# Kernel tuning notes

Hardware: AMD Instinct MI355X
Metric: run time of the kernel (lower is better)

Reference implementation:

```python
import jax, jax.numpy as jnp
import numpy as np

DIM = 512
NUM_HEADS = 8
HEAD_DIM = DIM // NUM_HEADS
FFN_DIM = 4 * DIM
EPS = 1e-6


def rmsnorm(x, w):
    rms = jnp.sqrt(jnp.mean(x * x, axis=-1, keepdims=True) + EPS)
    return x / rms * w


def setup_inputs() -> dict:
    key = jax.random.key(0)
    ks = jax.random.split(key, 8)
    B, T = 4, 2048
    x = jax.random.normal(ks[0], (B, T, DIM), dtype=jnp.float32)
    # Linear weights stored as [in, out] (transpose of torch layout)
    w_qkv = jax.random.normal(ks[1], (DIM, 3 * DIM), dtype=jnp.float32) * 0.02
    w_out = jax.random.normal(ks[2], (DIM, DIM), dtype=jnp.float32) * 0.02
    b_out = jnp.zeros((DIM,), dtype=jnp.float32)
    w1 = jax.random.normal(ks[3], (DIM, FFN_DIM), dtype=jnp.float32) * 0.02
    b1 = jnp.zeros((FFN_DIM,), dtype=jnp.float32)
    w2 = jax.random.normal(ks[4], (FFN_DIM, DIM), dtype=jnp.float32) * 0.02
    b2 = jnp.zeros((DIM,), dtype=jnp.float32)
    norm1_w = jnp.ones((DIM,), dtype=jnp.float32)
    norm2_w = jnp.ones((DIM,), dtype=jnp.float32)
    return {
        "x": x, "norm1_w": norm1_w, "norm2_w": norm2_w,
        "w_qkv": w_qkv, "w_out": w_out, "b_out": b_out,
        "w1": w1, "b1": b1, "w2": w2, "b2": b2,
        "context_size": 64,
    }


def reference(x, norm1_w, norm2_w, w_qkv, w_out, b_out, w1, b1, w2, b2, context_size):
    B, T, D = x.shape
    H, Hd = NUM_HEADS, HEAD_DIM
    # --- attention sublayer ---
    xn = rmsnorm(x, norm1_w)
    qkv = xn @ w_qkv                      # (B, T, 3D)
    q, k, v = jnp.split(qkv, 3, axis=-1)
    q = q.reshape(B, T, H, Hd).transpose(0, 2, 1, 3)  # (B, H, T, Hd)
    k = k.reshape(B, T, H, Hd).transpose(0, 2, 1, 3)
    v = v.reshape(B, T, H, Hd).transpose(0, 2, 1, 3)
    scale = Hd ** -0.5
    scores = jnp.einsum('bhqd,bhkd->bhqk', q, k) * scale  # (B, H, T, T)
    idx = jnp.arange(T)
    band = jnp.abs(idx[:, None] - idx[None, :]) <= context_size  # (T, T)
    scores = jnp.where(band[None, None], scores, -jnp.inf)
    attn = jax.nn.softmax(scores, axis=-1)
    out = jnp.einsum('bhqk,bhkd->bhqd', attn, v)  # (B, H, T, Hd)
    out = out.transpose(0, 2, 1, 3).reshape(B, T, D)
    out = out @ w_out + b_out
    x = x + out
    # --- FFN sublayer ---
    h = rmsnorm(x, norm2_w)
    h = jax.nn.gelu(h @ w1 + b1, approximate=False)
    x = x + (h @ w2 + b2)
    return x
```

## Files before the change

kernel.cpp:

```cpp
#include <hip/hip_runtime.h>
#include <cstdint>
#include <cstddef>

#define B_  4
#define T_  2048
#define D_  512
#define NH_ 8
#define HD_ 64
#define FF_ 2048
#define M_  (B_*T_)

typedef unsigned short u16;
typedef __attribute__((ext_vector_type(8))) unsigned short u16x8;
typedef __attribute__((ext_vector_type(8))) __bf16         bf16x8;
typedef __attribute__((ext_vector_type(4))) float          f32x4;

__device__ __forceinline__ u16 f2bf(float f) {
  unsigned u = __float_as_uint(f);
  u += 0x7FFF + ((u >> 16) & 1);
  return (u16)(u >> 16);
}
__device__ __forceinline__ float bf2f(u16 h) {
  return __uint_as_float((unsigned)h << 16);
}

__device__ __forceinline__ f32x4 mfma_bf16(u16x8 a, u16x8 b, f32x4 c) {
  return __builtin_amdgcn_mfma_f32_16x16x32_bf16(
      __builtin_bit_cast(bf16x8, a), __builtin_bit_cast(bf16x8, b), c, 0, 0, 0);
}

__device__ __forceinline__ void async16(const void* g, void* l) {
  __builtin_amdgcn_global_load_lds(
      (const __attribute__((address_space(1))) unsigned int*)g,
      (__attribute__((address_space(3))) unsigned int*)l, 16, 0, 0);
}

__device__ __forceinline__ float gelu_f(float v) {
  float ax = fabsf(v) * 0.70710678118f;
  float t = 1.0f / (1.0f + 0.3275911f * ax);
  float p = ((((1.061405429f * t - 1.453152027f) * t + 1.421413741f) * t
              - 0.284496736f) * t + 0.254829592f) * t;
  float e = __expf(-ax * ax);
  float er = 1.0f - p * e;
  float s = (v >= 0.0f) ? er : -er;
  return 0.5f * v * (1.0f + s);
}

__global__ __launch_bounds__(256) void trans4_kernel(
    const float* __restrict__ i0, u16* __restrict__ o0,
    const float* __restrict__ i1, u16* __restrict__ o1,
    const float* __restrict__ i2, u16* __restrict__ o2,
    const float* __restrict__ i3, u16* __restrict__ o3) {
  __shared__ float tile[32][33];
  int bid = blockIdx.x;
  const float* in; u16* out; int R, C, gx, lb;
  if (bid < 768)       { in = i0; out = o0; R = 512;  C = 1536; gx = 48; lb = bid; }
  else if (bid < 1024) { in = i1; out = o1; R = 512;  C = 512;  gx = 16; lb = bid - 768; }
  else if (bid < 2048) { in = i2; out = o2; R = 512;  C = 2048; gx = 64; lb = bid - 1024; }
  else                 { in = i3; out = o3; R = 2048; C = 512;  gx = 16; lb = bid - 2048; }
  int c0 = (lb % gx) * 32, r0 = (lb / gx) * 32;
  int tx = threadIdx.x, ty = threadIdx.y;
#pragma unroll
  for (int i = 0; i < 4; i++)
    tile[ty + i * 8][tx] = in[(size_t)(r0 + ty + i * 8) * C + c0 + tx];
  __syncthreads();
#pragma unroll
  for (int i = 0; i < 4; i++)
    out[(size_t)(c0 + ty + i * 8) * R + r0 + tx] = f2bf(tile[tx][ty + i * 8]);
}

template <bool INBF>
__global__ __launch_bounds__(256) void rmsnorm_kernel(const void* __restrict__ xv,
                                                      const float* __restrict__ w,
                                                      u16* __restrict__ out,
                                                      u16* __restrict__ rawout) {
  int row  = blockIdx.x * 4 + (threadIdx.x >> 6);
  int lane = threadIdx.x & 63;
  float v[8];
  if (INBF) {
    u16x8 raw = *(const u16x8*)((const u16*)xv + (size_t)row * D_ + lane * 8);
#pragma unroll
    for (int e = 0; e < 8; e++) v[e] = bf2f(raw[e]);
  } else {
    const float* xr = (const float*)xv + (size_t)row * D_ + lane * 8;
    *(float4*)(v)     = *(const float4*)xr;
    *(float4*)(v + 4) = *(const float4*)(xr + 4);
  }
  if (rawout) {
    u16 rw[8];
#pragma unroll
    for (int e = 0; e < 8; e++) rw[e] = f2bf(v[e]);
    *(uint4*)(rawout + (size_t)row * D_ + lane * 8) = *(uint4*)rw;
  }
  float ss = 0.f;
#pragma unroll
  for (int e = 0; e < 8; e++) ss += v[e] * v[e];
#pragma unroll
  for (int m = 1; m < 64; m <<= 1) ss += __shfl_xor(ss, m, 64);
  float inv = rsqrtf(ss * (1.0f / D_) + 1e-6f);
  const float* wr = w + lane * 8;
  float wv[8];
  *(float4*)(wv)     = *(const float4*)wr;
  *(float4*)(wv + 4) = *(const float4*)(wr + 4);
  u16 o[8];
#pragma unroll
  for (int e = 0; e < 8; e++) o[e] = f2bf(v[e] * inv * wv[e]);
  *(uint4*)(out + (size_t)row * D_ + lane * 8) = *(uint4*)o;
}

template <int BM, int BN, bool HAS_BIAS, int RES_MODE, bool DO_GELU, bool STORE_BF16>
__global__ __launch_bounds__(256) void gemm_kernel(
    const u16* __restrict__ A, const u16* __restrict__ Bt, void* __restrict__ Cv,
    const float* __restrict__ bias, const void* __restrict__ resv,
    int M, int N, int K) {
  constexpr int ACH = BM / 32;
  constexpr int BCH = BN / 32;
  constexpr int WM  = BM / 2, WN = BN / 2;
  constexpr int MI  = WM / 16, NJ = WN / 16;
  constexpr int EW  = BN + 4;
  constexpr int STG = (BM + BN) * 128;
  constexpr int EPB = 32 * EW * 4;
  constexpr int SMB = (2 * STG > EPB) ? 2 * STG : EPB;
  __shared__ __align__(16) char smem[SMB];
  const int tid = threadIdx.x;
  const int lane = tid & 63, w = tid >> 6;
  const int quad = lane >> 4, m16 = lane & 15;
  const int wm = w & 1, wn = w >> 1;
  const int m0 = blockIdx.y * BM, n0 = blockIdx.x * BN;

  f32x4 acc[MI][NJ];
#pragma unroll
  for (int i = 0; i < MI; i++)
#pragma unroll
    for (int j = 0; j < NJ; j++) acc[i][j] = (f32x4){0.f, 0.f, 0.f, 0.f};

  const int srow = tid >> 3;
  const int scol = (((tid & 7) ^ (srow & 7))) * 8;
  const u16* Ag = A  + (size_t)(m0 + srow) * K + scol;
  const u16* Bg = Bt + (size_t)(n0 + srow) * K + scol;

  auto stage = [&](int buf, int kt) {
    char* base = smem + buf * STG;
#pragma unroll
    for (int c = 0; c < ACH; c++)
      async16(Ag + (size_t)c * 32 * K + kt, base + c * 4096 + tid * 16);
#pragma unroll
    for (int c = 0; c < BCH; c++)
      async16(Bg + (size_t)c * 32 * K + kt, base + BM * 128 + c * 4096 + tid * 16);
  };
  auto compute = [&](int buf) {
    const u16* lA = (const u16*)(smem + buf * STG);
    const u16* lB = (const u16*)(smem + buf * STG + BM * 128);
#pragma unroll
    for (int kk = 0; kk < 2; kk++) {
      const int sl = ((kk * 4 + quad) ^ (m16 & 7)) * 8;
      const u16* pa = lA + (wm * WM + m16) * 64 + sl;
      const u16* pb = lB + (wn * WN + m16) * 64 + sl;
      u16x8 af[MI], bfr[NJ];
#pragma unroll
      for (int i = 0; i < MI; i++) af[i] = *(const u16x8*)(pa + i * 1024);
#pragma unroll
      for (int j = 0; j < NJ; j++) bfr[j] = *(const u16x8*)(pb + j * 1024);
#pragma unroll
      for (int i = 0; i < MI; i++)
#pragma unroll
        for (int j = 0; j < NJ; j++)
          acc[i][j] = mfma_bf16(af[i], bfr[j], acc[i][j]);
    }
  };

  const int nk = K >> 6;
  stage(0, 0);
  for (int t = 0; t < nk; t++) {
    __syncthreads();
    if (t + 1 < nk) stage((t + 1) & 1, (t + 1) << 6);
    compute(t & 1);
  }

  float* eps = (float*)smem;
  constexpr int REPS = (32 * BN) / (256 * 8);
  float bv[REPS > 0 ? REPS : 1][8];
  if (HAS_BIAS) {
#pragma unroll
    for (int rep = 0; rep < REPS; rep++) {
      const int col = (BN == 128) ? ((tid & 15) * 8) : ((tid & 7) * 8);
      *(float4*)(bv[rep])     = *(const float4*)(bias + n0 + col);
      *(float4*)(bv[rep] + 4) = *(const float4*)(bias + n0 + col + 4);
    }
  }
#pragma unroll
  for (int i = 0; i < MI; i++) {
    __syncthreads();
#pragma unroll
    for (int j = 0; j < NJ; j++)
#pragma unroll
      for (int r = 0; r < 4; r++)
        eps[(wm * 16 + quad * 4 + r) * EW + wn * WN + j * 16 + m16] =
            acc[i][j][r];
    __syncthreads();
#pragma unroll
    for (int rep = 0; rep < REPS; rep++) {
      const int lr  = (BN == 128) ? (rep * 16 + (tid >> 4)) : (tid >> 3);
      const int col = (BN == 128) ? ((tid & 15) * 8) : ((tid & 7) * 8);
      const int rg  = m0 + (lr >> 4) * WM + i * 16 + (lr & 15);
      float v[8];
      *(float4*)(v)     = *(const float4*)(eps + lr * EW + col);
      *(float4*)(v + 4) = *(const float4*)(eps + lr * EW + col + 4);
      if (HAS_BIAS) {
#pragma unroll
        for (int e = 0; e < 8; e++) v[e] += bv[rep][e];
      }
      if (DO_GELU) {
#pragma unroll
        for (int e = 0; e < 8; e++) v[e] = gelu_f(v[e]);
      }
      const size_t idx = (size_t)rg * N + n0 + col;
      if (RES_MODE == 1) {
        float4 r0 = *(const float4*)((const float*)resv + idx);
        float4 r1 = *(const float4*)((const float*)resv + idx + 4);
        v[0] += r0.x; v[1] += r0.y; v[2] += r0.z; v[3] += r0.w;
        v[4] += r1.x; v[5] += r1.y; v[6] += r1.z; v[7] += r1.w;
      } else if (RES_MODE == 2) {
        u16x8 rr = *(const u16x8*)((const u16*)resv + idx);
#pragma unroll
        for (int e = 0; e < 8; e++) v[e] += bf2f(rr[e]);
      }
      if (STORE_BF16) {
        u16 o[8];
#pragma unroll
        for (int e = 0; e < 8; e++) o[e] = f2bf(v[e]);
        *(uint4*)((u16*)Cv + idx) = *(uint4*)o;
      } else {
        *(float4*)((float*)Cv + idx)     = *(float4*)(v);
        *(float4*)((float*)Cv + idx + 4) = *(float4*)(v + 4);
      }
    }
  }
}

#define KP_ 72
#define VP_ 218
__global__ __launch_bounds__(256) void attn_kernel(const u16* __restrict__ qkv,
                                                   u16* __restrict__ out) {
  __shared__ __align__(16) char smem[29952 + 64 * VP_ * 2];
  u16* Ks = (u16*)smem;
  u16* Vt = (u16*)(smem + 29952);
  const int tid = threadIdx.x, lane = tid & 63, w = tid >> 6;
  const int quad = lane >> 4, m16 = lane & 15;
  const int q0 = blockIdx.x * 64, h = blockIdx.y, b = blockIdx.z;
  const int kstart = q0 - 64;
  const u16* base = qkv + (size_t)b * T_ * 1536;

  for (int c = tid; c < 1664; c += 256) {
    int row = c >> 3, cc = (c & 7) * 8;
    int j = kstart + row;
    j = j < 0 ? 0 : (j > T_ - 1 ? T_ - 1 : j);
    *(uint4*)(Ks + row * KP_ + cc) =
        *(const uint4*)(base + (size_t)j * 1536 + 512 + h * 64 + cc);
  }
  for (int c = tid; c < 1664; c += 256) {
    int row = c >> 3, cc = (c & 7) * 8;
    int j = kstart + row;
    j = j < 0 ? 0 : (j > T_ - 1 ? T_ - 1 : j);
    uint4 u = *(const uint4*)(base + (size_t)j * 1536 + 1024 + h * 64 + cc);
    u16 tmp[8];
    *(uint4*)tmp = u;
#pragma unroll
    for (int i = 0; i < 8; i++) Vt[(cc + i) * VP_ + row] = tmp[i];
  }
  const int qw = q0 + w * 16;
  const u16* qb = base + (size_t)(qw + m16) * 1536 + h * 64 + quad * 8;
  u16x8 a0 = *(const u16x8*)qb;
  u16x8 a1 = *(const u16x8*)(qb + 32);
  __syncthreads();

  float s[10][4];
#pragma unroll
  for (int t = 0; t < 10; t++) {
    int kt = (w + t) * 16;
    u16x8 kb0 = *(const u16x8*)(Ks + (kt + m16) * KP_ + quad * 8);
    u16x8 kb1 = *(const u16x8*)(Ks + (kt + m16) * KP_ + 32 + quad * 8);
    f32x4 acc = {0.f, 0.f, 0.f, 0.f};
    acc = mfma_bf16(a0, kb0, acc);
    acc = mfma_bf16(a1, kb1, acc);
    int jab = kstart + kt + m16;
#pragma unroll
    for (int r = 0; r < 4; r++) {
      int q = qw + quad * 4 + r;
      int d = q - jab;
      bool valid = (jab >= 0) && (jab < T_) && (d <= 64) && (d >= -64);
      s[t][r] = valid ? acc[r] * 0.125f : -1e30f;
    }
  }
  float mx[4], sm[4];
#pragma unroll
  for (int r = 0; r < 4; r++) mx[r] = -1e30f;
#pragma unroll
  for (int t = 0; t < 10; t++)
#pragma unroll
    for (int r = 0; r < 4; r++) mx[r] = fmaxf(mx[r], s[t][r]);
#pragma unroll
  for (int r = 0; r < 4; r++) {
#pragma unroll
    for (int msk = 1; msk < 16; msk <<= 1)
      mx[r] = fmaxf(mx[r], __shfl_xor(mx[r], msk, 64));
    sm[r] = 0.f;
  }
#pragma unroll
  for (int t = 0; t < 10; t++)
#pragma unroll
    for (int r = 0; r < 4; r++) {
      float e = __expf(s[t][r] - mx[r]);
      s[t][r] = e; sm[r] += e;
    }
#pragma unroll
  for (int r = 0; r < 4; r++) {
#pragma unroll
    for (int msk = 1; msk < 16; msk <<= 1) sm[r] += __shfl_xor(sm[r], msk, 64);
    sm[r] = 1.0f / sm[r];
  }
  __syncthreads();
  u16* Ps = (u16*)smem + w * 2688;
#pragma unroll
  for (int t = 0; t < 10; t++)
#pragma unroll
    for (int r = 0; r < 4; r++)
      Ps[(quad * 4 + r) * 168 + t * 16 + m16] = f2bf(s[t][r] * sm[r]);
  __syncthreads();

  f32x4 o[4];
#pragma unroll
  for (int dt = 0; dt < 4; dt++) o[dt] = (f32x4){0.f, 0.f, 0.f, 0.f};
#pragma unroll
  for (int c5 = 0; c5 < 5; c5++) {
    u16x8 pa = *(const u16x8*)(Ps + m16 * 168 + c5 * 32 + quad * 8);
#pragma unroll
    for (int dt = 0; dt < 4; dt++) {
      u16x8 vb = *(const u16x8*)(Vt + (dt * 16 + m16) * VP_ + w * 16 + c5 * 32 + quad * 8);
      o[dt] = mfma_bf16(pa, vb, o[dt]);
    }
  }
#pragma unroll
  for (int dt = 0; dt < 4; dt++)
#pragma unroll
    for (int r = 0; r < 4; r++)
      out[(size_t)(b * T_ + qw + quad * 4 + r) * D_ + h * HD_ + dt * 16 + m16] =
          f2bf(o[dt][r]);
}

extern "C" void kernel_launch(void* const* d_in, const int* in_sizes, int n_in,
                              void* d_out, int out_size, void* d_ws, size_t ws_size,
                              hipStream_t stream) {
  (void)in_sizes; (void)n_in; (void)out_size; (void)ws_size;
  const float* x     = (const float*)d_in[0];
  const float* n1w   = (const float*)d_in[1];
  const float* n2w   = (const float*)d_in[2];
  const float* w_qkv = (const float*)d_in[3];
  const float* w_out = (const float*)d_in[4];
  const float* b_out = (const float*)d_in[5];
  const float* w1    = (const float*)d_in[6];
  const float* b1    = (const float*)d_in[7];
  const float* w2    = (const float*)d_in[8];
  const float* b2    = (const float*)d_in[9];
  float* out = (float*)d_out;
  char* ws = (char*)d_ws;

  u16* wqkvT  = (u16*)(ws + 0);
  u16* woutT  = (u16*)(ws + 1572864);
  u16* w1T    = (u16*)(ws + 2097152);
  u16* w2T    = (u16*)(ws + 4194304);
  u16* xn     = (u16*)(ws + 6291456);
  u16* qkv    = (u16*)(ws + 14680064);
  u16* attno  = (u16*)(ws + 39845888);
  u16* x1     = (u16*)(ws + 48234496);
  u16* xbf    = (u16*)(ws + 56623104);
  u16* hn     = xn;
  u16* hbuf   = qkv;

  trans4_kernel<<<3072, dim3(32, 8), 0, stream>>>(
      w_qkv, wqkvT, w_out, woutT, w1, w1T, w2, w2T);

  rmsnorm_kernel<false><<<2048, 256, 0, stream>>>(x, n1w, xn, xbf);
  gemm_kernel<64, 128, false, 0, false, true><<<dim3(12, 128), 256, 0, stream>>>(
      xn, wqkvT, (void*)qkv, nullptr, nullptr, M_, 3 * D_, D_);
  attn_kernel<<<dim3(32, 8, 4), 256, 0, stream>>>(qkv, attno);
  gemm_kernel<64, 128, true, 2, false, true><<<dim3(4, 128), 256, 0, stream>>>(
      attno, woutT, (void*)x1, b_out, xbf, M_, D_, D_);
  rmsnorm_kernel<true><<<2048, 256, 0, stream>>>(x1, n2w, hn, nullptr);
  gemm_kernel<64, 128, true, 0, true, true><<<dim3(16, 128), 256, 0, stream>>>(
      hn, w1T, (void*)hbuf, b1, nullptr, M_, FF_, D_);
  gemm_kernel<64, 128, true, 2, false, false><<<dim3(4, 128), 256, 0, stream>>>(
      hbuf, w2T, (void*)out, b2, x1, M_, D_, FF_);
}
```

Measured before the change: 223.1 us.

## Merge weight transpose with first RMSNorm and enlarge QKV/FFN1 GEMM tiles

```diff
diff --git a/kernel.cpp b/kernel.cpp
--- a/kernel.cpp
+++ b/kernel.cpp
@@ -46,52 +46,67 @@
   return 0.5f * v * (1.0f + s);
 }
 
-__global__ __launch_bounds__(256) void trans4_kernel(
+__global__ __launch_bounds__(256) void prep_kernel(
     const float* __restrict__ i0, u16* __restrict__ o0,
     const float* __restrict__ i1, u16* __restrict__ o1,
     const float* __restrict__ i2, u16* __restrict__ o2,
-    const float* __restrict__ i3, u16* __restrict__ o3) {
+    const float* __restrict__ i3, u16* __restrict__ o3,
+    const float* __restrict__ x, const float* __restrict__ n1w,
+    u16* __restrict__ xn, u16* __restrict__ xbf) {
   __shared__ float tile[32][33];
-  int bid = blockIdx.x;
-  const float* in; u16* out; int R, C, gx, lb;
-  if (bid < 768)       { in = i0; out = o0; R = 512;  C = 1536; gx = 48; lb = bid; }
-  else if (bid < 1024) { in = i1; out = o1; R = 512;  C = 512;  gx = 16; lb = bid - 768; }
-  else if (bid < 2048) { in = i2; out = o2; R = 512;  C = 2048; gx = 64; lb = bid - 1024; }
-  else                 { in = i3; out = o3; R = 2048; C = 512;  gx = 16; lb = bid - 2048; }
-  int c0 = (lb % gx) * 32, r0 = (lb / gx) * 32;
-  int tx = threadIdx.x, ty = threadIdx.y;
-#pragma unroll
-  for (int i = 0; i < 4; i++)
-    tile[ty + i * 8][tx] = in[(size_t)(r0 + ty + i * 8) * C + c0 + tx];
-  __syncthreads();
-#pragma unroll
-  for (int i = 0; i < 4; i++)
-    out[(size_t)(c0 + ty + i * 8) * R + r0 + tx] = f2bf(tile[tx][ty + i * 8]);
-}
-
-template <bool INBF>
-__global__ __launch_bounds__(256) void rmsnorm_kernel(const void* __restrict__ xv,
+  const int bid = blockIdx.x, tid = threadIdx.x;
+  if (bid < 3072) {
+    const float* in; u16* out; int R, C, gx, lb;
+    if (bid < 768)       { in = i0; out = o0; R = 512;  C = 1536; gx = 48; lb = bid; }
+    else if (bid < 1024) { in = i1; out = o1; R = 512;  C = 512;  gx = 16; lb = bid - 768; }
+    else if (bid < 2048) { in = i2; out = o2; R = 512;  C = 2048; gx = 64; lb = bid - 1024; }
+    else                 { in = i3; out = o3; R = 2048; C = 512;  gx = 16; lb = bid - 2048; }
+    int c0 = (lb % gx) * 32, r0 = (lb / gx) * 32;
+    int tx = tid & 31, ty = tid >> 5;
+#pragma unroll
+    for (int i = 0; i < 4; i++)
+      tile[ty + i * 8][tx] = in[(size_t)(r0 + ty + i * 8) * C + c0 + tx];
+    __syncthreads();
+#pragma unroll
+    for (int i = 0; i < 4; i++)
+      out[(size_t)(c0 + ty + i * 8) * R + r0 + tx] = f2bf(tile[tx][ty + i * 8]);
+  } else {
+    int row  = (bid - 3072) * 4 + (tid >> 6);
+    int lane = tid & 63;
+    const float* xr = x + (size_t)row * D_ + lane * 8;
+    float v[8];
+    *(float4*)(v)     = *(const float4*)xr;
+    *(float4*)(v + 4) = *(const float4*)(xr + 4);
+    u16 rw[8];
+#pragma unroll
+    for (int e = 0; e < 8; e++) rw[e] = f2bf(v[e]);
+    *(uint4*)(xbf + (size_t)row * D_ + lane * 8) = *(uint4*)rw;
+    float ss = 0.f;
+#pragma unroll
+    for (int e = 0; e < 8; e++) ss += v[e] * v[e];
+#pragma unroll
+    for (int m = 1; m < 64; m <<= 1) ss += __shfl_xor(ss, m, 64);
+    float inv = rsqrtf(ss * (1.0f / D_) + 1e-6f);
+    const float* wr = n1w + lane * 8;
+    float wv[8];
+    *(float4*)(wv)     = *(const float4*)wr;
+    *(float4*)(wv + 4) = *(const float4*)(wr + 4);
+    u16 o[8];
+#pragma unroll
+    for (int e = 0; e < 8; e++) o[e] = f2bf(v[e] * inv * wv[e]);
+    *(uint4*)(xn + (size_t)row * D_ + lane * 8) = *(uint4*)o;
+  }
+}
+
+__global__ __launch_bounds__(256) void rmsnorm_kernel(const u16* __restrict__ xv,
                                                       const float* __restrict__ w,
-                                                      u16* __restrict__ out,
-                                                      u16* __restrict__ rawout) {
+                                                      u16* __restrict__ out) {
   int row  = blockIdx.x * 4 + (threadIdx.x >> 6);
   int lane = threadIdx.x & 63;
   float v[8];
-  if (INBF) {
-    u16x8 raw = *(const u16x8*)((const u16*)xv + (size_t)row * D_ + lane * 8);
-#pragma unroll
-    for (int e = 0; e < 8; e++) v[e] = bf2f(raw[e]);
-  } else {
-    const float* xr = (const float*)xv + (size_t)row * D_ + lane * 8;
-    *(float4*)(v)     = *(const float4*)xr;
-    *(float4*)(v + 4) = *(const float4*)(xr + 4);
-  }
-  if (rawout) {
-    u16 rw[8];
-#pragma unroll
-    for (int e = 0; e < 8; e++) rw[e] = f2bf(v[e]);
-    *(uint4*)(rawout + (size_t)row * D_ + lane * 8) = *(uint4*)rw;
-  }
+  u16x8 raw = *(const u16x8*)(xv + (size_t)row * D_ + lane * 8);
+#pragma unroll
+  for (int e = 0; e < 8; e++) v[e] = bf2f(raw[e]);
   float ss = 0.f;
 #pragma unroll
   for (int e = 0; e < 8; e++) ss += v[e] * v[e];
@@ -377,17 +392,16 @@
   u16* hn     = xn;
   u16* hbuf   = qkv;
 
-  trans4_kernel<<<3072, dim3(32, 8), 0, stream>>>(
-      w_qkv, wqkvT, w_out, woutT, w1, w1T, w2, w2T);
-
-  rmsnorm_kernel<false><<<2048, 256, 0, stream>>>(x, n1w, xn, xbf);
-  gemm_kernel<64, 128, false, 0, false, true><<<dim3(12, 128), 256, 0, stream>>>(
+  prep_kernel<<<5120, 256, 0, stream>>>(
+      w_qkv, wqkvT, w_out, woutT, w1, w1T, w2, w2T, x, n1w, xn, xbf);
+
+  gemm_kernel<128, 128, false, 0, false, true><<<dim3(12, 64), 256, 0, stream>>>(
       xn, wqkvT, (void*)qkv, nullptr, nullptr, M_, 3 * D_, D_);
   attn_kernel<<<dim3(32, 8, 4), 256, 0, stream>>>(qkv, attno);
   gemm_kernel<64, 128, true, 2, false, true><<<dim3(4, 128), 256, 0, stream>>>(
       attno, woutT, (void*)x1, b_out, xbf, M_, D_, D_);
-  rmsnorm_kernel<true><<<2048, 256, 0, stream>>>(x1, n2w, hn, nullptr);
-  gemm_kernel<64, 128, true, 0, true, true><<<dim3(16, 128), 256, 0, stream>>>(
+  rmsnorm_kernel<<<2048, 256, 0, stream>>>(x1, n2w, hn);
+  gemm_kernel<128, 128, true, 0, true, true><<<dim3(16, 64), 256, 0, stream>>>(
       hn, w1T, (void*)hbuf, b1, nullptr, M_, FF_, D_);
   gemm_kernel<64, 128, true, 2, false, false><<<dim3(4, 128), 256, 0, stream>>>(
       hbuf, w2T, (void*)out, b2, x1, M_, D_, FF_);
```

Result: no change. 222.4 us (-0.3%).
